# Kernel optimization log

Hardware: AMD Instinct MI355X
Metric: run time of the kernel (lower is better)

Reference implementation:

```python
import math
import jax, jax.numpy as jnp
import numpy as np

B = 8
NUM_POINTS = 4096
LATENT = 512
HID = 512
AD = 128
R1, R2, R_ATT = 1.0, 1.5, 0.2
EPS = 1e-5
SQRT_D = math.sqrt(AD)


def _fibonacci_sphere_points(n, radius):
    if n <= 0:
        return np.zeros((0, 3), np.float32)
    i = np.arange(n, dtype=np.float32)
    phi = (1 + 5 ** 0.5) / 2
    theta = 2 * math.pi * i / phi
    z = 1.0 - 2.0 * (i + 0.5) / n
    r_xy = np.sqrt(np.maximum(1.0 - z * z, 0.0))
    return (radius * np.stack((r_xy * np.cos(theta), r_xy * np.sin(theta), z), axis=-1)).astype(np.float32)


def _make_template():
    n_shell = NUM_POINTS - 1
    area_ratio = R1 ** 2 / (R1 ** 2 + R2 ** 2)
    n1 = max(1, round(n_shell * area_ratio))
    n2 = n_shell - n1
    if n2 == 0:
        n1, n2 = n1 - 1, 1
    t1 = _fibonacci_sphere_points(n1, R1)
    t2 = _fibonacci_sphere_points(n2, R2)
    return jnp.asarray(np.concatenate([np.zeros((1, 3), np.float32), t1, t2], axis=0))


def setup_inputs() -> dict:
    key = jax.random.key(0)
    ks = iter(jax.random.split(key, 64))
    d = {}
    d['z'] = jax.random.normal(next(ks), (B, LATENT), jnp.float32)
    d['template'] = _make_template()
    d['wq'] = jax.random.normal(next(ks), (AD, 3), jnp.float32) * 0.1
    d['wk'] = jax.random.normal(next(ks), (AD, 3), jnp.float32) * 0.1
    d['wv'] = jax.random.normal(next(ks), (AD, 3), jnp.float32) * 0.1
    in_dims = [LATENT + 3, LATENT + 3 + AD, LATENT + 3 + AD]
    for s, in_dim in enumerate(in_dims):
        d[f's{s}_w1'] = jax.random.normal(next(ks), (HID, in_dim), jnp.float32) * (1.0 / math.sqrt(in_dim))
        d[f's{s}_b1'] = jnp.zeros((HID,), jnp.float32)
        d[f's{s}_g1'] = jnp.ones((HID,), jnp.float32)
        d[f's{s}_be1'] = jnp.zeros((HID,), jnp.float32)
        d[f's{s}_w2'] = jax.random.normal(next(ks), (HID, HID), jnp.float32) * (1.0 / math.sqrt(HID))
        d[f's{s}_b2'] = jnp.zeros((HID,), jnp.float32)
        d[f's{s}_g2'] = jnp.ones((HID,), jnp.float32)
        d[f's{s}_be2'] = jnp.zeros((HID,), jnp.float32)
        d[f's{s}_w3'] = jax.random.normal(next(ks), (3, HID), jnp.float32) * (1.0 / math.sqrt(HID))
        d[f's{s}_b3'] = jnp.zeros((3,), jnp.float32)
    return d


def _bn_relu(x, gamma, beta):
    # BatchNorm1d in training mode over channel dim of (B, N, C): stats over (B, N)
    mean = jnp.mean(x, axis=(0, 1))
    var = jnp.var(x, axis=(0, 1))
    xn = (x - mean) * jax.lax.rsqrt(var + EPS)
    return jax.nn.relu(xn * gamma + beta)


def _stage(x, w1, b1, g1, be1, w2, b2, g2, be2, w3, b3):
    h = _bn_relu(x @ w1.T + b1, g1, be1)
    h = _bn_relu(h @ w2.T + b2, g2, be2)
    return h @ w3.T + b3


def _local_attention(coords, wq, wk, wv):
    Q = coords @ wq.T  # (B, N, AD)
    K = coords @ wk.T
    V = coords @ wv.T
    sq = jnp.sum(coords * coords, axis=-1)  # (B, N)
    D2 = sq[:, :, None] + sq[:, None, :] - 2.0 * jnp.einsum('bnd,bmd->bnm', coords, coords)
    mask = D2 <= R_ATT ** 2  # diagonal always True (D2=0)
    scores = jnp.einsum('bnd,bmd->bnm', Q, K) / SQRT_D
    scores = jnp.where(mask, scores, -jnp.inf)
    W = jax.nn.softmax(scores, axis=-1)
    W = jnp.where(mask, W, 0.0)
    return jnp.einsum('bnm,bmd->bnd', W, V)


def reference(z, template, wq, wk, wv,
              s0_w1, s0_b1, s0_g1, s0_be1, s0_w2, s0_b2, s0_g2, s0_be2, s0_w3, s0_b3,
              s1_w1, s1_b1, s1_g1, s1_be1, s1_w2, s1_b2, s1_g2, s1_be2, s1_w3, s1_b3,
              s2_w1, s2_b1, s2_g1, s2_be1, s2_w2, s2_b2, s2_g2, s2_be2, s2_w3, s2_b3):
    Bz = z.shape[0]
    z_exp = jnp.broadcast_to(z[:, None, :], (Bz, NUM_POINTS, LATENT))
    tmpl = jnp.broadcast_to(template[None], (Bz, NUM_POINTS, 3))
    coords0 = _stage(jnp.concatenate((z_exp, tmpl), axis=-1),
                     s0_w1, s0_b1, s0_g1, s0_be1, s0_w2, s0_b2, s0_g2, s0_be2, s0_w3, s0_b3)
    attn1 = _local_attention(coords0, wq, wk, wv)
    coords1 = _stage(jnp.concatenate((z_exp, coords0, attn1), axis=-1),
                     s1_w1, s1_b1, s1_g1, s1_be1, s1_w2, s1_b2, s1_g2, s1_be2, s1_w3, s1_b3)
    attn2 = _local_attention(coords1, wq, wk, wv)
    coords2 = _stage(jnp.concatenate((z_exp, coords1, attn2), axis=-1),
                     s2_w1, s2_b1, s2_g1, s2_be1, s2_w2, s2_b2, s2_g2, s2_be2, s2_w3, s2_b3)
    return coords2
```

## Files before the change

### kernel.cpp

```cpp
#include <hip/hip_runtime.h>
#include <math.h>

#define NPTS 4096
#define BATCH 8
#define HIDD 512
#define ROWS 32768
#define R_ATT2 0.04f
#define INV_SQRT_D 0.08838834764831845f
#define LOG2E 1.4426950408889634f

typedef unsigned short u16;
typedef unsigned int u32;
typedef __attribute__((ext_vector_type(8))) short s8v;
typedef __attribute__((ext_vector_type(4))) float f4v;
typedef __attribute__((ext_vector_type(4))) u32 u4v;
typedef __attribute__((ext_vector_type(2))) u32 u2v;

__device__ __forceinline__ float u2f(u16 v) { return __uint_as_float(((u32)v) << 16); }
__device__ __forceinline__ u16 f2u(float f) {
  u32 u = __float_as_uint(f);
  return (u16)((u + 0x7fffu + ((u >> 16) & 1u)) >> 16);
}
__device__ __forceinline__ u32 packtrunc(float x0, float x1) {
  return (__float_as_uint(x1) & 0xFFFF0000u) | (__float_as_uint(x0) >> 16);
}
__device__ __forceinline__ float fast_exp2(float x) {
  float r;
  asm("v_exp_f32 %0, %1" : "=v"(r) : "v"(x));
  return r;
}
__device__ __forceinline__ s8v mk8(u32 a, u32 b, u32 c, u32 d) {
  union { u4v u; s8v s; } x;
  x.u = (u4v){a, b, c, d};
  return x.s;
}

__global__ void gram_k(const float* __restrict__ wq, const float* __restrict__ wk,
                       float* __restrict__ G) {
  int ab = threadIdx.x;
  if (ab < 9) {
    int a = ab / 3, b = ab % 3;
    float s = 0.f;
    for (int d = 0; d < 128; ++d) s = fmaf(wq[d * 3 + a], wk[d * 3 + b], s);
    G[ab] = s;
  }
}

__global__ __launch_bounds__(256) void prep2_k(
    const float* __restrict__ z, const float* __restrict__ w1, int ldw,
    const float* __restrict__ b1, const float* __restrict__ w2,
    float* __restrict__ zwbuf, float* __restrict__ ubuf,
    u16* __restrict__ w1abf, u16* __restrict__ w2bf, int doW1a) {
  int wid = blockIdx.x * 4 + (threadIdx.x >> 6);
  int lane = threadIdx.x & 63;
  {
    int b = wid >> 9, c = wid & 511;
    const float* zr = z + b * 512;
    const float* wr = w1 + (size_t)c * ldw;
    float acc = 0.f;
#pragma unroll
    for (int k = lane; k < 512; k += 64) acc = fmaf(zr[k], wr[k], acc);
#pragma unroll
    for (int off = 32; off; off >>= 1) acc += __shfl_down(acc, off);
    if (lane == 0) zwbuf[wid] = acc + b1[c];
  }
  int idx = blockIdx.x * 256 + threadIdx.x;
  if (idx < 1536) {
    int a = idx >> 9, c = idx & 511;
    ubuf[idx] = w1[(size_t)c * ldw + 512 + a];
  }
  if (doW1a && idx < 65536) {
    int n = idx >> 7, k = idx & 127;
    w1abf[idx] = f2u(w1[(size_t)n * 643 + 515 + k]);
  }
  w2bf[idx] = f2u(w2[idx]);
}

__global__ __launch_bounds__(256) void s0l1s_k(const float* __restrict__ tmpl,
                                               const float* __restrict__ u,
                                               const float* __restrict__ zw,
                                               u16* __restrict__ h,
                                               float* __restrict__ psum,
                                               float* __restrict__ psumsq) {
  __shared__ float Ls[4][512];
  __shared__ float Lq[4][512];
  int g = blockIdx.x;
  int wave = threadIdx.x >> 6, lane = threadIdx.x & 63;
  int b = g >> 8;
  int c0 = lane * 8;
  const float* zr = zw + b * 512 + c0;
  const float* u0 = u + c0;
  const float* u1 = u + 512 + c0;
  const float* u2 = u + 1024 + c0;
  float zv[8], u0v[8], u1v[8], u2v[8];
#pragma unroll
  for (int j = 0; j < 8; ++j) {
    zv[j] = zr[j]; u0v[j] = u0[j]; u1v[j] = u1[j]; u2v[j] = u2[j];
  }
  float s[8] = {0, 0, 0, 0, 0, 0, 0, 0}, q[8] = {0, 0, 0, 0, 0, 0, 0, 0};
  int row0 = g * 16 + wave * 4;
#pragma unroll
  for (int t = 0; t < 4; ++t) {
    int row = row0 + t;
    int n = row & (NPTS - 1);
    float tx = tmpl[n * 3], ty = tmpl[n * 3 + 1], tz = tmpl[n * 3 + 2];
    u32 outw[4];
#pragma unroll
    for (int jj = 0; jj < 4; ++jj) {
      float v0 = zv[2 * jj] + tx * u0v[2 * jj] + ty * u1v[2 * jj] + tz * u2v[2 * jj];
      float v1 = zv[2 * jj + 1] + tx * u0v[2 * jj + 1] + ty * u1v[2 * jj + 1] + tz * u2v[2 * jj + 1];
      outw[jj] = packtrunc(v0, v1);
      float r0 = u2f((u16)(outw[jj] & 0xffffu));
      float r1 = u2f((u16)(outw[jj] >> 16));
      s[2 * jj] += r0;     q[2 * jj] = fmaf(r0, r0, q[2 * jj]);
      s[2 * jj + 1] += r1; q[2 * jj + 1] = fmaf(r1, r1, q[2 * jj + 1]);
    }
    *(uint4*)(h + (size_t)row * 512 + c0) = *(const uint4*)outw;
  }
#pragma unroll
  for (int j = 0; j < 8; ++j) {
    Ls[wave][c0 + j] = s[j];
    Lq[wave][c0 + j] = q[j];
  }
  __syncthreads();
  int c2 = threadIdx.x * 2;
#pragma unroll
  for (int cc = 0; cc < 2; ++cc) {
    int c = c2 + cc;
    psum[g * 512 + c] = Ls[0][c] + Ls[1][c] + Ls[2][c] + Ls[3][c];
    psumsq[g * 512 + c] = Lq[0][c] + Lq[1][c] + Lq[2][c] + Lq[3][c];
  }
}

__global__ __launch_bounds__(256) void bnrelu_k(u16* __restrict__ h,
                                                const float* __restrict__ sc,
                                                const float* __restrict__ sh) {
  int nthreads = gridDim.x * 256;
  int total = ROWS * 512 / 8;
  for (int i = blockIdx.x * 256 + threadIdx.x; i < total; i += nthreads) {
    int k0 = (i * 8) & 511;
    uint4 v = *(const uint4*)(h + (size_t)i * 8);
    const u16* p = (const u16*)&v;
    u32 outw[4];
#pragma unroll
    for (int t = 0; t < 4; ++t) {
      float x0 = fmaxf(fmaf(u2f(p[2 * t]), sc[k0 + 2 * t], sh[k0 + 2 * t]), 0.f);
      float x1 = fmaxf(fmaf(u2f(p[2 * t + 1]), sc[k0 + 2 * t + 1], sh[k0 + 2 * t + 1]), 0.f);
      outw[t] = packtrunc(x0, x1);
    }
    *(uint4*)(h + (size_t)i * 8) = *(const uint4*)outw;
  }
}

template <bool MODE1>
__global__ __launch_bounds__(256) void gemm_mfma_k(
    const u16* __restrict__ A, int lda, const u16* __restrict__ B, int ldb, int K,
    const float* __restrict__ bias, const float* __restrict__ zw,
    const float* __restrict__ u, const float4* __restrict__ c4,
    u16* __restrict__ C, float* __restrict__ psum, float* __restrict__ psumsq) {
  __shared__ u16 As[128 * 32];
  __shared__ u16 Bs[128 * 32];
  int tid = threadIdx.x;
  int wave = tid >> 6, lane = tid & 63;
  int quad = lane >> 4, l16 = lane & 15;
  int m0 = blockIdx.x * 128, n0 = blockIdx.y * 128;
  int wm = (wave & 1) * 64, wn = (wave >> 1) * 64;
  int srow0 = lane >> 2;
  int sc8 = (lane & 3) * 8;
  f4v acc[4][4];
#pragma unroll
  for (int mi = 0; mi < 4; ++mi)
#pragma unroll
    for (int ni = 0; ni < 4; ++ni) acc[mi][ni] = (f4v){0.f, 0.f, 0.f, 0.f};

  for (int k0 = 0; k0 < K; k0 += 32) {
#pragma unroll
    for (int j = 0; j < 2; ++j) {
      int chunk = wave * 2 + j;
      int row = chunk * 16 + srow0;
      const u16* gA = A + (size_t)(m0 + row) * lda + k0 + sc8;
      const u16* gB = B + (size_t)(n0 + row) * ldb + k0 + sc8;
      __builtin_amdgcn_global_load_lds(
          (const __attribute__((address_space(1))) void*)gA,
          (__attribute__((address_space(3))) void*)(As + chunk * 512), 16, 0, 0);
      __builtin_amdgcn_global_load_lds(
          (const __attribute__((address_space(1))) void*)gB,
          (__attribute__((address_space(3))) void*)(Bs + chunk * 512), 16, 0, 0);
    }
    __syncthreads();
    s8v af[4], bfv[4];
#pragma unroll
    for (int mi = 0; mi < 4; ++mi)
      af[mi] = *(const s8v*)&As[(wm + mi * 16 + l16) * 32 + quad * 8];
#pragma unroll
    for (int ni = 0; ni < 4; ++ni)
      bfv[ni] = *(const s8v*)&Bs[(wn + ni * 16 + l16) * 32 + quad * 8];
#pragma unroll
    for (int mi = 0; mi < 4; ++mi)
#pragma unroll
      for (int ni = 0; ni < 4; ++ni)
        acc[mi][ni] = __builtin_amdgcn_mfma_f32_16x16x32_bf16(
            af[mi], bfv[ni], acc[mi][ni], 0, 0, 0);
    __syncthreads();
  }

  int batch = m0 >> 12;
  float e0[4], e1[4], e2[4], e3[4];
  float ps[4] = {0, 0, 0, 0}, pq[4] = {0, 0, 0, 0};
#pragma unroll
  for (int ni = 0; ni < 4; ++ni) {
    int gn = n0 + wn + ni * 16 + l16;
    if (MODE1) {
      e0[ni] = zw[batch * 512 + gn];
      e1[ni] = u[gn];
      e2[ni] = u[512 + gn];
      e3[ni] = u[1024 + gn];
    } else {
      e0[ni] = bias[gn];
    }
  }
#pragma unroll
  for (int mi = 0; mi < 4; ++mi) {
#pragma unroll
    for (int reg = 0; reg < 4; ++reg) {
      int gm = m0 + wm + mi * 16 + quad * 4 + reg;
      float cx = 0.f, cy = 0.f, cz = 0.f;
      if (MODE1) {
        float4 p = c4[gm];
        cx = p.x; cy = p.y; cz = p.z;
      }
#pragma unroll
      for (int ni = 0; ni < 4; ++ni) {
        int gn = n0 + wn + ni * 16 + l16;
        float v = acc[mi][ni][reg] + e0[ni];
        if (MODE1) v += cx * e1[ni] + cy * e2[ni] + cz * e3[ni];
        u16 r = f2u(v);
        C[(size_t)gm * 512 + gn] = r;
        float vr = u2f(r);
        ps[ni] += vr;
        pq[ni] = fmaf(vr, vr, pq[ni]);
      }
    }
  }
  float* Lps = (float*)As;
  float* Lpq = (float*)Bs;
#pragma unroll
  for (int ni = 0; ni < 4; ++ni) {
    Lps[((wave * 4 + quad) * 4 + ni) * 16 + l16] = ps[ni];
    Lpq[((wave * 4 + quad) * 4 + ni) * 16 + l16] = pq[ni];
  }
  __syncthreads();
  if (tid < 128) {
    int wn2 = tid >> 6, rem = tid & 63;
    int nni = rem >> 4, ll = rem & 15;
    int gn = n0 + wn2 * 64 + nni * 16 + ll;
    float s = 0.f, q = 0.f;
#pragma unroll
    for (int wv = 0; wv < 2; ++wv)
#pragma unroll
      for (int qd = 0; qd < 4; ++qd) {
        int w2 = wn2 * 2 + wv;
        s += Lps[((w2 * 4 + qd) * 4 + nni) * 16 + ll];
        q += Lpq[((w2 * 4 + qd) * 4 + nni) * 16 + ll];
      }
    psum[(size_t)blockIdx.x * 512 + gn] = s;
    psumsq[(size_t)blockIdx.x * 512 + gn] = q;
  }
}

__global__ __launch_bounds__(256) void bn_fin_k(
    const float* __restrict__ psum, const float* __restrict__ psumsq, int nslabs,
    const float* __restrict__ gamma, const float* __restrict__ beta,
    float* __restrict__ sc, float* __restrict__ sh) {
  int c = blockIdx.x * 4 + (threadIdx.x >> 6);
  int lane = threadIdx.x & 63;
  float s = 0.f, q = 0.f;
  for (int g = lane; g < nslabs; g += 64) {
    s += psum[g * 512 + c];
    q += psumsq[g * 512 + c];
  }
#pragma unroll
  for (int off = 32; off; off >>= 1) {
    s += __shfl_down(s, off);
    q += __shfl_down(q, off);
  }
  if (lane == 0) {
    float mean = s * (1.f / 32768.f);
    float var = fmaxf(q * (1.f / 32768.f) - mean * mean, 0.f);
    float inv = rsqrtf(var + 1e-5f);
    float scale = gamma[c] * inv;
    sc[c] = scale;
    sh[c] = beta[c] - mean * scale;
  }
}

__global__ __launch_bounds__(256) void l3_k(const u16* __restrict__ h,
                                            const float* __restrict__ sc,
                                            const float* __restrict__ sh,
                                            const float* __restrict__ w3,
                                            const float* __restrict__ b3,
                                            float4* __restrict__ c4out,
                                            float* __restrict__ fout) {
  int wid = blockIdx.x * 4 + (threadIdx.x >> 6);
  int lane = threadIdx.x & 63;
  int k0 = lane * 8;
  uint4 hv = *(const uint4*)(h + (size_t)wid * 512 + k0);
  const u16* hp = (const u16*)&hv;
  float a0 = 0, a1 = 0, a2 = 0;
#pragma unroll
  for (int j = 0; j < 8; ++j) {
    int k = k0 + j;
    float x = fmaxf(fmaf(u2f(hp[j]), sc[k], sh[k]), 0.f);
    a0 = fmaf(x, w3[k], a0);
    a1 = fmaf(x, w3[512 + k], a1);
    a2 = fmaf(x, w3[1024 + k], a2);
  }
#pragma unroll
  for (int off = 32; off; off >>= 1) {
    a0 += __shfl_down(a0, off);
    a1 += __shfl_down(a1, off);
    a2 += __shfl_down(a2, off);
  }
  if (lane == 0) {
    a0 += b3[0]; a1 += b3[1]; a2 += b3[2];
    if (c4out) {
      float sq = a0 * a0 + a1 * a1 + a2 * a2;
      c4out[wid] = make_float4(a0, a1, a2, sq);
    }
    if (fout) {
      fout[(size_t)wid * 3 + 0] = a0;
      fout[(size_t)wid * 3 + 1] = a1;
      fout[(size_t)wid * 3 + 2] = a2;
    }
  }
}

__global__ __launch_bounds__(256) void cprep_k(const float4* __restrict__ c4,
                                               u4v* __restrict__ frag,
                                               u16* __restrict__ ctg) {
  int i = blockIdx.x * 256 + threadIdx.x;
  float4 p = c4[i];
  float nhw = -0.5f * p.w;
  u16 hx = f2u(p.x), hy = f2u(p.y), hz = f2u(p.z), hw = f2u(nhw);
  u16 lx = f2u(p.x - u2f(hx)), ly = f2u(p.y - u2f(hy));
  u16 lz = f2u(p.z - u2f(hz)), lw = f2u(nhw - u2f(hw));
  u32 h01 = (u32)hx | ((u32)hy << 16), h23 = (u32)hz | ((u32)hw << 16);
  u32 l01 = (u32)lx | ((u32)ly << 16), l23 = (u32)lz | ((u32)lw << 16);
  frag[i] = (u4v){h01, h23, l01, l23};
  int chunk = i >> 5, p32 = i & 31;
  u16* base = ctg + (size_t)chunk * 128;
  base[p32] = 0x3F80;
  base[32 + p32] = hx;
  base[64 + p32] = hy;
  base[96 + p32] = hz;
}

__global__ __launch_bounds__(512) void attnm_k(const float4* __restrict__ c4,
                                               const u4v* __restrict__ frag,
                                               const u16* __restrict__ ctg,
                                               const float* __restrict__ G,
                                               const float* __restrict__ wv,
                                               u16* __restrict__ attnb) {
  __shared__ __align__(16) char lds[65536 + 8192];
  int wave = threadIdx.x >> 6, lane = threadIdx.x & 63;
  int g = lane >> 4, q16 = lane & 15;
  int qbase = blockIdx.x * 64;
  int b = qbase >> 12;
  int pt0 = wave * 512;
  char* ebufW = lds + wave * 8192;
  float* fin = (float*)(lds + 65536);
  int chunk0 = b * 128 + (pt0 >> 5);

  float Gr[9];
#pragma unroll
  for (int i = 0; i < 9; ++i) Gr[i] = G[i];
  u32 bh0[4], bh1[4], bh2[4], bh3[4];
  u32 sh0[4], sh1[4], sh2[4], sh3[4];
  float thr[4];
#pragma unroll
  for (int s = 0; s < 4; ++s) {
    float4 cq = c4[qbase + s * 16 + q16];
    thr[s] = 0.5f * (cq.w - R_ATT2);
    u16 hx = f2u(cq.x), hy = f2u(cq.y), hz = f2u(cq.z);
    u16 lx = f2u(cq.x - u2f(hx)), ly = f2u(cq.y - u2f(hy)), lz = f2u(cq.z - u2f(hz));
    u32 h01 = (u32)hx | ((u32)hy << 16);
    u32 h23 = (u32)hz | (0x3F80u << 16);
    u32 l01 = (u32)lx | ((u32)ly << 16);
    u32 l23 = (u32)lz;
    bh0[s] = (g <= 1) ? h01 : 0u;
    bh1[s] = (g <= 1) ? h23 : 0u;
    bh2[s] = (g == 0) ? l01 : 0u;
    bh3[s] = (g == 0) ? l23 : 0u;
    const float SC = INV_SQRT_D * LOG2E;
    float g0v = (cq.x * Gr[0] + cq.y * Gr[3] + cq.z * Gr[6]) * SC;
    float g1v = (cq.x * Gr[1] + cq.y * Gr[4] + cq.z * Gr[7]) * SC;
    float g2v = (cq.x * Gr[2] + cq.y * Gr[5] + cq.z * Gr[8]) * SC;
    u16 ghx = f2u(g0v), ghy = f2u(g1v), ghz = f2u(g2v);
    u16 glx = f2u(g0v - u2f(ghx)), gly = f2u(g1v - u2f(ghy)), glz = f2u(g2v - u2f(ghz));
    u32 gh01 = (u32)ghx | ((u32)ghy << 16);
    u32 gh23 = (u32)ghz;
    u32 gl01 = (u32)glx | ((u32)gly << 16);
    u32 gl23 = (u32)glz;
    sh0[s] = (g <= 1) ? gh01 : 0u;
    sh1[s] = (g <= 1) ? gh23 : 0u;
    sh2[s] = (g == 0) ? gl01 : 0u;
    sh3[s] = (g == 0) ? gl23 : 0u;
  }

  f4v pvAcc[4];
#pragma unroll
  for (int s = 0; s < 4; ++s) pvAcc[s] = (f4v){0.f, 0.f, 0.f, 0.f};

  int csw = g ^ (q16 & 3);
  for (int w = 0; w < 16; ++w) {
    char* ebuf = ebufW + (w & 1) * 4096;
#pragma unroll
    for (int tp = 0; tp < 2; ++tp) {
      int p = pt0 + w * 32 + tp * 16 + q16;
      u4v f = frag[(size_t)b * NPTS + p];
      u32 a0 = (g == 0) ? f.x : ((g == 1) ? f.z : 0u);
      u32 a1 = (g == 0) ? f.y : ((g == 1) ? f.w : 0u);
      u32 a2 = (g == 0) ? f.x : 0u;
      u32 a3 = (g == 0) ? f.y : 0u;
      s8v av = mk8(a0, a1, a2, a3);
      int wsw = ((tp * 2 + (g >> 1)) ^ (q16 & 3)) * 16 + (g & 1) * 8;
#pragma unroll
      for (int s = 0; s < 4; ++s) {
        f4v z4 = (f4v){0.f, 0.f, 0.f, 0.f};
        f4v dmv = __builtin_amdgcn_mfma_f32_16x16x32_bf16(
            av, mk8(bh0[s], bh1[s], bh2[s], bh3[s]), z4, 0, 0, 0);
        f4v s2v = __builtin_amdgcn_mfma_f32_16x16x32_bf16(
            av, mk8(sh0[s], sh1[s], sh2[s], sh3[s]), z4, 0, 0, 0);
        float e0 = (dmv[0] >= thr[s]) ? fast_exp2(s2v[0]) : 0.f;
        float e1 = (dmv[1] >= thr[s]) ? fast_exp2(s2v[1]) : 0.f;
        float e2 = (dmv[2] >= thr[s]) ? fast_exp2(s2v[2]) : 0.f;
        float e3 = (dmv[3] >= thr[s]) ? fast_exp2(s2v[3]) : 0.f;
        u2v ew = (u2v){packtrunc(e0, e1), packtrunc(e2, e3)};
        *(u2v*)(ebuf + s * 1024 + q16 * 64 + wsw) = ew;
      }
    }
    const u16* ctb = ctg + (size_t)(chunk0 + w) * 128 + (q16 & 3) * 32 + g * 8;
    u4v bt = *(const u4v*)ctb;
    s8v pvB = mk8(bt.x, bt.y, bt.z, bt.w);
#pragma unroll
    for (int s = 0; s < 4; ++s) {
      u4v at = *(const u4v*)(ebuf + s * 1024 + q16 * 64 + csw * 16);
      pvAcc[s] = __builtin_amdgcn_mfma_f32_16x16x32_bf16(
          mk8(at.x, at.y, at.z, at.w), pvB, pvAcc[s], 0, 0, 0);
    }
  }

  if (q16 < 4) {
#pragma unroll
    for (int s = 0; s < 4; ++s)
#pragma unroll
      for (int r = 0; r < 4; ++r)
        fin[wave * 256 + (s * 16 + g * 4 + r) * 4 + q16] = pvAcc[s][r];
  }
  __syncthreads();
  float* comb = (float*)lds;
  int t = threadIdx.x;
  if (t < 256) {
    int qb = t >> 2, c = t & 3;
    float acc = 0.f;
#pragma unroll
    for (int wv8 = 0; wv8 < 8; ++wv8) acc += fin[wv8 * 256 + qb * 4 + c];
    comb[qb * 4 + c] = acc;
  }
  __syncthreads();
#pragma unroll
  for (int it = 0; it < 8; ++it) {
    int task = t + it * 512;
    int qb = task >> 6, dp = task & 63;
    float sw = comb[qb * 4 + 0];
    float sx = comb[qb * 4 + 1];
    float sy = comb[qb * 4 + 2];
    float sz = comb[qb * 4 + 3];
    float inv = 1.f / sw;
    float ox = sx * inv, oy = sy * inv, oz = sz * inv;
    int d0 = dp * 2;
    float v0 = ox * wv[d0 * 3] + oy * wv[d0 * 3 + 1] + oz * wv[d0 * 3 + 2];
    float v1 = ox * wv[d0 * 3 + 3] + oy * wv[d0 * 3 + 4] + oz * wv[d0 * 3 + 5];
    u32 pack = (u32)f2u(v0) | ((u32)f2u(v1) << 16);
    *(u32*)(attnb + (size_t)(qbase + qb) * 128 + d0) = pack;
  }
}

extern "C" void kernel_launch(void* const* d_in, const int* in_sizes, int n_in,
                              void* d_out, int out_size, void* d_ws, size_t ws_size,
                              hipStream_t stream) {
  const float* z = (const float*)d_in[0];
  const float* tmpl = (const float*)d_in[1];
  const float* wq = (const float*)d_in[2];
  const float* wk = (const float*)d_in[3];
  const float* wv = (const float*)d_in[4];
  const float* sw[3][10];
  for (int s = 0; s < 3; ++s)
    for (int j = 0; j < 10; ++j) sw[s][j] = (const float*)d_in[5 + s * 10 + j];

  char* base = (char*)d_ws;
  size_t off = 0;
  auto alloc = [&](size_t bytes) -> void* {
    void* p = base + off;
    off = (off + bytes + 255) & ~(size_t)255;
    return p;
  };
  u16* hA = (u16*)alloc((size_t)ROWS * 512 * 2);
  u16* hB = (u16*)alloc((size_t)ROWS * 512 * 2);
  u16* attnb = (u16*)alloc((size_t)ROWS * 128 * 2);
  float4* c4 = (float4*)alloc((size_t)ROWS * 16);
  float* psum = (float*)alloc(2048 * 512 * 4);
  float* psumsq = (float*)alloc(2048 * 512 * 4);
  float* zwbuf = (float*)alloc(4096 * 4);
  float* scv = (float*)alloc(512 * 4);
  float* shv = (float*)alloc(512 * 4);
  float* G = (float*)alloc(256);
  u16* w1abf = (u16*)alloc(512 * 128 * 2);
  u16* w2bf = (u16*)alloc(512 * 512 * 2);
  float* ubuf = (float*)alloc(1536 * 4);
  u4v* fragb = (u4v*)alloc((size_t)ROWS * 16);
  u16* ctg = (u16*)alloc((size_t)1024 * 128 * 2);

  gram_k<<<1, 64, 0, stream>>>(wq, wk, G);

  for (int s = 0; s < 3; ++s) {
    int ldw = (s == 0) ? 515 : 643;
    prep2_k<<<1024, 256, 0, stream>>>(z, sw[s][0], ldw, sw[s][1], sw[s][4],
                                      zwbuf, ubuf, w1abf, w2bf, s == 0 ? 0 : 1);
    if (s == 0) {
      s0l1s_k<<<2048, 256, 0, stream>>>(tmpl, ubuf, zwbuf, hA, psum, psumsq);
      bn_fin_k<<<128, 256, 0, stream>>>(psum, psumsq, 2048,
                                        sw[s][2], sw[s][3], scv, shv);
    } else {
      gemm_mfma_k<true><<<dim3(256, 4), 256, 0, stream>>>(
          attnb, 128, w1abf, 128, 128, nullptr, zwbuf, ubuf, c4,
          hA, psum, psumsq);
      bn_fin_k<<<128, 256, 0, stream>>>(psum, psumsq, 256,
                                        sw[s][2], sw[s][3], scv, shv);
    }
    bnrelu_k<<<2048, 256, 0, stream>>>(hA, scv, shv);
    gemm_mfma_k<false><<<dim3(256, 4), 256, 0, stream>>>(
        hA, 512, w2bf, 512, 512, sw[s][5], nullptr, nullptr, nullptr,
        hB, psum, psumsq);
    bn_fin_k<<<128, 256, 0, stream>>>(psum, psumsq, 256,
                                      sw[s][6], sw[s][7], scv, shv);
    bool last = (s == 2);
    l3_k<<<8192, 256, 0, stream>>>(hB, scv, shv, sw[s][8], sw[s][9],
                                   last ? nullptr : c4,
                                   last ? (float*)d_out : nullptr);
    if (!last) {
      cprep_k<<<128, 256, 0, stream>>>(c4, fragb, ctg);
      attnm_k<<<512, 512, 0, stream>>>(c4, fragb, ctg, G, wv, attnb);
    }
  }
}
```

Baseline: 466.7 us.

## Double-buffer LDS tiles in the MFMA GEMM to overlap loads with compute

The MFMA GEMM kernel now uses two LDS buffers for the A and B tiles. It issues the async global-to-LDS loads for the next K-slice before running the MFMAs on the current one. This cuts the barriers per K iteration from two to one and hides global load latency behind the matrix math. In exchange LDS use per block doubles, which may lower occupancy, and correctness depends on the barrier waiting for the outstanding async LDS loads.

```diff
diff --git a/kernel.cpp b/kernel.cpp
--- a/kernel.cpp
+++ b/kernel.cpp
@@ -158,8 +158,8 @@
     const float* __restrict__ bias, const float* __restrict__ zw,
     const float* __restrict__ u, const float4* __restrict__ c4,
     u16* __restrict__ C, float* __restrict__ psum, float* __restrict__ psumsq) {
-  __shared__ u16 As[128 * 32];
-  __shared__ u16 Bs[128 * 32];
+  __shared__ u16 As[2][128 * 32];
+  __shared__ u16 Bs[2][128 * 32];
   int tid = threadIdx.x;
   int wave = tid >> 6, lane = tid & 63;
   int quad = lane >> 4, l16 = lane & 15;
@@ -173,28 +173,41 @@
 #pragma unroll
     for (int ni = 0; ni < 4; ++ni) acc[mi][ni] = (f4v){0.f, 0.f, 0.f, 0.f};
 
-  for (int k0 = 0; k0 < K; k0 += 32) {
-#pragma unroll
-    for (int j = 0; j < 2; ++j) {
-      int chunk = wave * 2 + j;
-      int row = chunk * 16 + srow0;
-      const u16* gA = A + (size_t)(m0 + row) * lda + k0 + sc8;
-      const u16* gB = B + (size_t)(n0 + row) * ldb + k0 + sc8;
-      __builtin_amdgcn_global_load_lds(
-          (const __attribute__((address_space(1))) void*)gA,
-          (__attribute__((address_space(3))) void*)(As + chunk * 512), 16, 0, 0);
-      __builtin_amdgcn_global_load_lds(
-          (const __attribute__((address_space(1))) void*)gB,
-          (__attribute__((address_space(3))) void*)(Bs + chunk * 512), 16, 0, 0);
-    }
-    __syncthreads();
+  int chunk = wave * 2;
+  int row0 = chunk * 16 + srow0;
+  const u16* gA0 = A + (size_t)(m0 + row0) * lda + sc8;
+  const u16* gA1 = A + (size_t)(m0 + row0 + 16) * lda + sc8;
+  const u16* gB0 = B + (size_t)(n0 + row0) * ldb + sc8;
+  const u16* gB1 = B + (size_t)(n0 + row0 + 16) * ldb + sc8;
+
+  auto stage = [&](int nb, int k0) {
+    __builtin_amdgcn_global_load_lds(
+        (const __attribute__((address_space(1))) void*)(gA0 + k0),
+        (__attribute__((address_space(3))) void*)(As[nb] + chunk * 512), 16, 0, 0);
+    __builtin_amdgcn_global_load_lds(
+        (const __attribute__((address_space(1))) void*)(gA1 + k0),
+        (__attribute__((address_space(3))) void*)(As[nb] + (chunk + 1) * 512), 16, 0, 0);
+    __builtin_amdgcn_global_load_lds(
+        (const __attribute__((address_space(1))) void*)(gB0 + k0),
+        (__attribute__((address_space(3))) void*)(Bs[nb] + chunk * 512), 16, 0, 0);
+    __builtin_amdgcn_global_load_lds(
+        (const __attribute__((address_space(1))) void*)(gB1 + k0),
+        (__attribute__((address_space(3))) void*)(Bs[nb] + (chunk + 1) * 512), 16, 0, 0);
+  };
+
+  int NT = K >> 5;
+  stage(0, 0);
+  __syncthreads();
+  int cur = 0;
+  for (int t = 0; t < NT; ++t) {
+    if (t + 1 < NT) stage(cur ^ 1, (t + 1) * 32);
     s8v af[4], bfv[4];
 #pragma unroll
     for (int mi = 0; mi < 4; ++mi)
-      af[mi] = *(const s8v*)&As[(wm + mi * 16 + l16) * 32 + quad * 8];
+      af[mi] = *(const s8v*)&As[cur][(wm + mi * 16 + l16) * 32 + quad * 8];
 #pragma unroll
     for (int ni = 0; ni < 4; ++ni)
-      bfv[ni] = *(const s8v*)&Bs[(wn + ni * 16 + l16) * 32 + quad * 8];
+      bfv[ni] = *(const s8v*)&Bs[cur][(wn + ni * 16 + l16) * 32 + quad * 8];
 #pragma unroll
     for (int mi = 0; mi < 4; ++mi)
 #pragma unroll
@@ -202,6 +215,7 @@
         acc[mi][ni] = __builtin_amdgcn_mfma_f32_16x16x32_bf16(
             af[mi], bfv[ni], acc[mi][ni], 0, 0, 0);
     __syncthreads();
+    cur ^= 1;
   }
 
   int batch = m0 >> 12;
```

After: 461.2 us. Within noise of the previous version (-1.2%).
